# Kernel tuning notes

Hardware: AMD Instinct MI355X
Metric: run time of the kernel (lower is better)

## Reference

```python
import jax, jax.numpy as jnp
import numpy as np

C_IN, C_HID, N_HEADS = 128, 32, 4
INF = 1.0e9
LN_EPS = 1e-5


def setup_inputs() -> dict:
    key = jax.random.key(0)
    ks = jax.random.split(key, 12)
    B, I, J, C, H, D = 1, 384, 384, C_IN, N_HEADS, C_HID
    s = 0.02
    return {
        "x": jax.random.normal(ks[0], (B, I, J, C), dtype=jnp.float32),
        "mask": jnp.ones((B, I, J), dtype=jnp.float32),
        "ln_g": jnp.ones((C,), dtype=jnp.float32),
        "ln_b": jnp.zeros((C,), dtype=jnp.float32),
        "w_tri": jax.random.normal(ks[1], (C, H), dtype=jnp.float32) * s,
        "wq": jax.random.normal(ks[2], (C, H, D), dtype=jnp.float32) * s,
        "wk": jax.random.normal(ks[3], (C, H, D), dtype=jnp.float32) * s,
        "wv": jax.random.normal(ks[4], (C, H, D), dtype=jnp.float32) * s,
        "wg": jax.random.normal(ks[5], (C, H, D), dtype=jnp.float32) * s,
        "bg": jnp.ones((H, D), dtype=jnp.float32),
        "wo": jax.random.normal(ks[6], (H, D, C), dtype=jnp.float32) * s,
        "bo": jnp.zeros((C,), dtype=jnp.float32),
    }


def reference(x, mask, ln_g, ln_b, w_tri, wq, wk, wv, wg, bg, wo, bo):
    # LayerNorm over channel dim
    mu = jnp.mean(x, axis=-1, keepdims=True)
    var = jnp.mean(jnp.square(x - mu), axis=-1, keepdims=True)
    xn = (x - mu) * jax.lax.rsqrt(var + LN_EPS) * ln_g + ln_b  # [B,I,J,C]

    # mask bias: [B, I, 1, 1, J]
    mask_bias = (INF * (mask - 1.0))[..., :, None, None, :]
    # triangle bias: linear(x) -> [B,I,J,H] -> [B,1,H,I,J]
    tri_bias = jnp.einsum("bijc,ch->bhij", xn, w_tri)[:, None]

    scale = 1.0 / jnp.sqrt(jnp.asarray(C_HID, dtype=xn.dtype))
    # per-row attention over J: tensors [B, I, H, J, D]
    q = jnp.einsum("bixc,chd->bihxd", xn, wq) * scale
    k = jnp.einsum("bixc,chd->bihxd", xn, wk)
    v = jnp.einsum("bixc,chd->bihxd", xn, wv)

    logits = jnp.einsum("bihqd,bihkd->bihqk", q, k) + mask_bias + tri_bias
    a = jax.nn.softmax(logits, axis=-1)
    o = jnp.einsum("bihqk,bihkd->bihqd", a, v)  # [B,I,H,J,D]

    g = jax.nn.sigmoid(jnp.einsum("bixc,chd->bihxd", xn, wg) + bg[None, None, :, None, :])
    o = o * g
    out = jnp.einsum("bihxd,hdc->bixc", o, wo) + bo  # [B,I,J,C]
    return out
```

## Files before the change

### kernel.cpp

```cpp
#include <hip/hip_runtime.h>
#include <math.h>


#define I_DIM 384
#define J_DIM 384
#define C_DIM 128
#define H_DIM 4
#define D_DIM 32
#define NPOS (I_DIM * J_DIM)
#define Q_SCALE 0.17677669529663687f

typedef __attribute__((ext_vector_type(8))) short bf16x8;
typedef __attribute__((ext_vector_type(4))) float f32x4;

__device__ __forceinline__ float sigmoidf_(float v) {
    return 1.0f / (1.0f + __expf(-v));
}
__device__ __forceinline__ unsigned short f2bf(float f) {
    union { float f; unsigned u; } x; x.f = f;
    unsigned u = x.u;
    u += 0x7fffu + ((u >> 16) & 1u);
    return (unsigned short)(u >> 16);
}
__device__ __forceinline__ float bf2f(unsigned short v) {
    union { unsigned u; float f; } x; x.u = ((unsigned)v) << 16;
    return x.f;
}

__global__ __launch_bounds__(256) void prep_kernel(
    const float* __restrict__ wq, const float* __restrict__ wk,
    const float* __restrict__ wv, const float* __restrict__ wg,
    const float* __restrict__ wo, unsigned short* __restrict__ Wt)
{
    const int mat = blockIdx.x;
    const float* W = (mat == 0) ? wq : (mat == 1) ? wk : (mat == 2) ? wv
                    : (mat == 3) ? wg : wo;
    const float scale = (mat == 0) ? Q_SCALE : 1.0f;
    const int t = threadIdx.x;
    const int n = t >> 1, c0 = (t & 1) * 64;
#pragma unroll
    for (int u = 0; u < 8; ++u) {
        unsigned pk[4];
#pragma unroll
        for (int w = 0; w < 4; ++w) {
            const unsigned short a = f2bf(W[(size_t)(c0 + u * 8 + w * 2 + 0) * 128 + n] * scale);
            const unsigned short b = f2bf(W[(size_t)(c0 + u * 8 + w * 2 + 1) * 128 + n] * scale);
            pk[w] = (unsigned)a | ((unsigned)b << 16);
        }
        int4 q; q.x = pk[0]; q.y = pk[1]; q.z = pk[2]; q.w = pk[3];
        *(int4*)(Wt + (size_t)mat * 16384 + n * 128 + c0 + u * 8) = q;
    }
}

__global__ __launch_bounds__(256) void proj_kernel(
    const float* __restrict__ x, const float* __restrict__ ln_g,
    const float* __restrict__ ln_b, const float* __restrict__ w_tri,
    const unsigned short* __restrict__ Wt, const float* __restrict__ bg,
    unsigned short* __restrict__ qb, unsigned short* __restrict__ kb,
    unsigned short* __restrict__ vb, unsigned short* __restrict__ gb,
    float* __restrict__ tri)
{
    __shared__ unsigned short At[128 * 128];
    __shared__ unsigned short Bt[128 * 128];

    const int t = threadIdx.x;
    const int pos0 = blockIdx.x * 128;
    const int lane = t & 63, wave = t >> 6;
    const int q15 = lane & 15, quad = lane >> 4;

    {
        const int r = t >> 1, half = t & 1, c0 = half * 64;
        const float* xrow = x + (size_t)(pos0 + r) * C_DIM + c0;
        float xv[64];
        float s = 0.f, ss = 0.f;
#pragma unroll
        for (int u = 0; u < 16; ++u) {
            float4 v4 = ((const float4*)xrow)[u];
            xv[u * 4 + 0] = v4.x; xv[u * 4 + 1] = v4.y;
            xv[u * 4 + 2] = v4.z; xv[u * 4 + 3] = v4.w;
            s  += v4.x + v4.y + v4.z + v4.w;
            ss += v4.x * v4.x + v4.y * v4.y + v4.z * v4.z + v4.w * v4.w;
        }
        s  += __shfl_xor(s, 1);
        ss += __shfl_xor(ss, 1);
        const float mu  = s * (1.0f / 128.0f);
        const float var = ss * (1.0f / 128.0f) - mu * mu;
        const float rstd = rsqrtf(var + 1e-5f);

        float ptri[4] = {0.f, 0.f, 0.f, 0.f};
#pragma unroll
        for (int u = 0; u < 8; ++u) {
            const float4 g0 = ((const float4*)(ln_g + c0))[u * 2];
            const float4 g1 = ((const float4*)(ln_g + c0))[u * 2 + 1];
            const float4 b0 = ((const float4*)(ln_b + c0))[u * 2];
            const float4 b1 = ((const float4*)(ln_b + c0))[u * 2 + 1];
            float xn8[8];
            xn8[0] = (xv[u * 8 + 0] - mu) * rstd * g0.x + b0.x;
            xn8[1] = (xv[u * 8 + 1] - mu) * rstd * g0.y + b0.y;
            xn8[2] = (xv[u * 8 + 2] - mu) * rstd * g0.z + b0.z;
            xn8[3] = (xv[u * 8 + 3] - mu) * rstd * g0.w + b0.w;
            xn8[4] = (xv[u * 8 + 4] - mu) * rstd * g1.x + b1.x;
            xn8[5] = (xv[u * 8 + 5] - mu) * rstd * g1.y + b1.y;
            xn8[6] = (xv[u * 8 + 6] - mu) * rstd * g1.z + b1.z;
            xn8[7] = (xv[u * 8 + 7] - mu) * rstd * g1.w + b1.w;
#pragma unroll
            for (int w = 0; w < 8; ++w) {
                const float4 wt = ((const float4*)w_tri)[c0 + u * 8 + w];
                ptri[0] += xn8[w] * wt.x; ptri[1] += xn8[w] * wt.y;
                ptri[2] += xn8[w] * wt.z; ptri[3] += xn8[w] * wt.w;
            }
            unsigned pk[4];
#pragma unroll
            for (int w = 0; w < 4; ++w)
                pk[w] = (unsigned)f2bf(xn8[w * 2]) | ((unsigned)f2bf(xn8[w * 2 + 1]) << 16);
            int4 q4; q4.x = pk[0]; q4.y = pk[1]; q4.z = pk[2]; q4.w = pk[3];
            const int c = half * 8 + u;
            *(int4*)&At[r * 128 + ((c ^ (r & 7)) * 8)] = q4;
        }
#pragma unroll
        for (int hh = 0; hh < 4; ++hh) ptri[hh] += __shfl_xor(ptri[hh], 1);
        const int pos = pos0 + r;
        const int i = pos / J_DIM, j = pos - (pos / J_DIM) * J_DIM;
        const int h0 = half * 2;
        tri[((size_t)(h0 + 0) * J_DIM + j) * I_DIM + i] = ptri[h0 + 0];
        tri[((size_t)(h0 + 1) * J_DIM + j) * I_DIM + i] = ptri[h0 + 1];
    }

    const int m0 = wave * 32;
    for (int mat = 0; mat < 4; ++mat) {
        __syncthreads();
        {
            const int rn = t >> 1, half = t & 1;
            const unsigned short* src = Wt + (size_t)mat * 16384 + rn * 128 + half * 64;
#pragma unroll
            for (int u = 0; u < 8; ++u) {
                const int c = half * 8 + u;
                *(int4*)&Bt[rn * 128 + ((c ^ (rn & 7)) * 8)] = *(const int4*)(src + u * 8);
            }
        }
        __syncthreads();

        f32x4 acc[2][8];
#pragma unroll
        for (int mt = 0; mt < 2; ++mt)
#pragma unroll
            for (int nt = 0; nt < 8; ++nt) acc[mt][nt] = (f32x4){0.f, 0.f, 0.f, 0.f};

#pragma unroll
        for (int kk = 0; kk < 4; ++kk) {
            const int sw = ((kk * 4 + quad) ^ (q15 & 7)) * 8;
            const bf16x8 a0 = *(const bf16x8*)&At[(m0 + q15) * 128 + sw];
            const bf16x8 a1 = *(const bf16x8*)&At[(m0 + 16 + q15) * 128 + sw];
#pragma unroll
            for (int nt = 0; nt < 8; ++nt) {
                const bf16x8 b = *(const bf16x8*)&Bt[(nt * 16 + q15) * 128 + sw];
                acc[0][nt] = __builtin_amdgcn_mfma_f32_16x16x32_bf16(a0, b, acc[0][nt], 0, 0, 0);
                acc[1][nt] = __builtin_amdgcn_mfma_f32_16x16x32_bf16(a1, b, acc[1][nt], 0, 0, 0);
            }
        }

        __syncthreads();
#pragma unroll
        for (int mt = 0; mt < 2; ++mt)
#pragma unroll
            for (int nt = 0; nt < 8; ++nt) {
                const int col = nt * 16 + q15;
                const float bgl = (mat == 3) ? bg[col] : 0.f;
#pragma unroll
                for (int reg = 0; reg < 4; ++reg) {
                    float v = acc[mt][nt][reg];
                    if (mat == 3) v = sigmoidf_(v + bgl);
                    const int row = m0 + mt * 16 + quad * 4 + reg;
                    Bt[row * 128 + (((col >> 3) ^ (row & 7)) * 8) + (col & 7)] = f2bf(v);
                }
            }
        __syncthreads();
        {
            unsigned short* O = (mat == 0) ? qb : (mat == 1) ? kb : (mat == 2) ? vb : gb;
#pragma unroll
            for (int sgm = 0; sgm < 2; ++sgm) {
                const int ch = t + sgm * 256;
                const int r = ch >> 2, hh = ch & 3;
                const int pos = pos0 + r;
                const int i = pos / J_DIM, j = pos - (pos / J_DIM) * J_DIM;
                unsigned short* dst = O + (((size_t)i * H_DIM + hh) * J_DIM + j) * D_DIM;
#pragma unroll
                for (int w = 0; w < 4; ++w) {
                    const int c = hh * 4 + w;
                    *(int4*)(dst + w * 8) = *(const int4*)&Bt[r * 128 + ((c ^ (r & 7)) * 8)];
                }
            }
        }
    }
}

__global__ __launch_bounds__(256) void attn_kernel(
    const unsigned short* __restrict__ qb, const unsigned short* __restrict__ kb,
    const unsigned short* __restrict__ vb, unsigned short* gob,
    const float* __restrict__ triT, const float* __restrict__ mask)
{
    __shared__ unsigned short Klds[64 * 32];
    __shared__ unsigned short Vt[32 * 68];
    __shared__ unsigned short Plds[4][32 * 68];
    __shared__ float Mb[J_DIM];

    const int t = threadIdx.x;
    const int lane = t & 63, wave = t >> 6;
    const int q15 = lane & 15, quad = lane >> 4;
    const int i = blockIdx.x >> 2, h = blockIdx.x & 3;
    const size_t hb = (size_t)(i * H_DIM + h) * (J_DIM * D_DIM);
    const int m0 = wave * 96;

    for (int idx = t; idx < J_DIM; idx += 256)
        Mb[idx] = 1.0e9f * (mask[i * J_DIM + idx] - 1.0f);

    bf16x8 qf[6];
#pragma unroll
    for (int m = 0; m < 6; ++m)
        qf[m] = *(const bf16x8*)(qb + hb + (size_t)(m0 + m * 16 + q15) * D_DIM + quad * 8);

    f32x4 Oacc[6][2];
    float sums[6][4];
#pragma unroll
    for (int m = 0; m < 6; ++m) {
#pragma unroll
        for (int d2 = 0; d2 < 2; ++d2) Oacc[m][d2] = (f32x4){0.f, 0.f, 0.f, 0.f};
#pragma unroll
        for (int r = 0; r < 4; ++r) sums[m][r] = 0.f;
    }

    unsigned short* Pw = Plds[wave];
    const float* triH = triT + (size_t)h * J_DIM * I_DIM;

    for (int kt = 0; kt < 6; ++kt) {
        __syncthreads();
        {
            const int kp = t >> 2, du = (t & 3) * 8;
            const size_t gsrc = hb + (size_t)(kt * 64 + kp) * D_DIM + du;
            *(int4*)&Klds[kp * 32 + du] = *(const int4*)(kb + gsrc);
            int4 vv = *(const int4*)(vb + gsrc);
            const unsigned short* vs = (const unsigned short*)&vv;
#pragma unroll
            for (int u = 0; u < 8; ++u)
                Vt[(du + u) * 68 + kp] = vs[u];
        }
        __syncthreads();

        bf16x8 vf[2][2];
#pragma unroll
        for (int ks = 0; ks < 2; ++ks)
#pragma unroll
            for (int d2 = 0; d2 < 2; ++d2)
                vf[ks][d2] = *(const bf16x8*)&Vt[(d2 * 16 + q15) * 68 + ks * 32 + quad * 8];

#pragma unroll
        for (int pass = 0; pass < 3; ++pass) {
            const int mbase = pass * 2;

#pragma unroll
            for (int nt = 0; nt < 4; ++nt) {
                const bf16x8 kf = *(const bf16x8*)&Klds[(nt * 16 + q15) * 32 + quad * 8];
                const float mb = Mb[kt * 64 + nt * 16 + q15];
                const float* tcol = triH + (size_t)(kt * 64 + nt * 16 + q15) * I_DIM;
#pragma unroll
                for (int mm = 0; mm < 2; ++mm) {
                    const int m = mbase + mm;
                    const float4 tb = *(const float4*)(tcol + m0 + m * 16 + quad * 4);
                    f32x4 s = {0.f, 0.f, 0.f, 0.f};
                    s = __builtin_amdgcn_mfma_f32_16x16x32_bf16(qf[m], kf, s, 0, 0, 0);
                    const float p0 = __expf(s[0] + mb + tb.x);
                    const float p1 = __expf(s[1] + mb + tb.y);
                    const float p2 = __expf(s[2] + mb + tb.z);
                    const float p3 = __expf(s[3] + mb + tb.w);
                    sums[m][0] += p0; sums[m][1] += p1;
                    sums[m][2] += p2; sums[m][3] += p3;
                    const int row = mm * 16 + quad * 4;
                    const int col = nt * 16 + q15;
                    Pw[(row + 0) * 68 + col] = f2bf(p0);
                    Pw[(row + 1) * 68 + col] = f2bf(p1);
                    Pw[(row + 2) * 68 + col] = f2bf(p2);
                    Pw[(row + 3) * 68 + col] = f2bf(p3);
                }
            }

#pragma unroll
            for (int mm = 0; mm < 2; ++mm) {
                const int m = mbase + mm;
#pragma unroll
                for (int ks = 0; ks < 2; ++ks) {
                    const bf16x8 af = *(const bf16x8*)&Pw[(mm * 16 + q15) * 68 + ks * 32 + quad * 8];
                    Oacc[m][0] = __builtin_amdgcn_mfma_f32_16x16x32_bf16(af, vf[ks][0], Oacc[m][0], 0, 0, 0);
                    Oacc[m][1] = __builtin_amdgcn_mfma_f32_16x16x32_bf16(af, vf[ks][1], Oacc[m][1], 0, 0, 0);
                }
            }
        }
    }

    float inv[6][4];
#pragma unroll
    for (int m = 0; m < 6; ++m)
#pragma unroll
        for (int r = 0; r < 4; ++r) {
            float s0 = sums[m][r];
            s0 += __shfl_xor(s0, 1); s0 += __shfl_xor(s0, 2);
            s0 += __shfl_xor(s0, 4); s0 += __shfl_xor(s0, 8);
            inv[m][r] = 1.0f / s0;
        }

#pragma unroll
    for (int m = 0; m < 6; ++m) {
        const int qrow = m0 + m * 16 + quad * 4;
#pragma unroll
        for (int d2 = 0; d2 < 2; ++d2) {
            const int d = d2 * 16 + q15;
#pragma unroll
            for (int r = 0; r < 4; ++r) {
                const size_t idx = hb + (size_t)(qrow + r) * D_DIM + d;
                const float g = bf2f(gob[idx]);
                gob[idx] = f2bf(Oacc[m][d2][r] * inv[m][r] * g);
            }
        }
    }
}

__global__ __launch_bounds__(256) void out_kernel(
    const unsigned short* __restrict__ og, const unsigned short* __restrict__ WtO,
    const float* __restrict__ bo, float* __restrict__ out)
{
    __shared__ unsigned short At[128 * 128];
    __shared__ unsigned short Bt[128 * 128];

    const int t = threadIdx.x;
    const int pos0 = blockIdx.x * 128;
    const int lane = t & 63, wave = t >> 6;
    const int q15 = lane & 15, quad = lane >> 4;

    {
        const int r = t >> 1, half = t & 1;
        const int pos = pos0 + r;
        const int i = pos / J_DIM, j = pos - (pos / J_DIM) * J_DIM;
#pragma unroll
        for (int u = 0; u < 8; ++u) {
            const int k0 = half * 64 + u * 8;
            const int hh = k0 >> 5, d0 = k0 & 31;
            const int4 v = *(const int4*)(og + (((size_t)i * H_DIM + hh) * J_DIM + j) * D_DIM + d0);
            const int c = half * 8 + u;
            *(int4*)&At[r * 128 + ((c ^ (r & 7)) * 8)] = v;
        }
        const unsigned short* src = WtO + r * 128 + half * 64;
#pragma unroll
        for (int u = 0; u < 8; ++u) {
            const int c = half * 8 + u;
            *(int4*)&Bt[r * 128 + ((c ^ (r & 7)) * 8)] = *(const int4*)(src + u * 8);
        }
    }
    __syncthreads();

    const int m0 = wave * 32;
    f32x4 acc[2][8];
#pragma unroll
    for (int mt = 0; mt < 2; ++mt)
#pragma unroll
        for (int nt = 0; nt < 8; ++nt) acc[mt][nt] = (f32x4){0.f, 0.f, 0.f, 0.f};

#pragma unroll
    for (int kk = 0; kk < 4; ++kk) {
        const int sw = ((kk * 4 + quad) ^ (q15 & 7)) * 8;
        const bf16x8 a0 = *(const bf16x8*)&At[(m0 + q15) * 128 + sw];
        const bf16x8 a1 = *(const bf16x8*)&At[(m0 + 16 + q15) * 128 + sw];
#pragma unroll
        for (int nt = 0; nt < 8; ++nt) {
            const bf16x8 b = *(const bf16x8*)&Bt[(nt * 16 + q15) * 128 + sw];
            acc[0][nt] = __builtin_amdgcn_mfma_f32_16x16x32_bf16(a0, b, acc[0][nt], 0, 0, 0);
            acc[1][nt] = __builtin_amdgcn_mfma_f32_16x16x32_bf16(a1, b, acc[1][nt], 0, 0, 0);
        }
    }

#pragma unroll
    for (int mt = 0; mt < 2; ++mt)
#pragma unroll
        for (int nt = 0; nt < 8; ++nt) {
            const float bov = bo[nt * 16 + q15];
#pragma unroll
            for (int reg = 0; reg < 4; ++reg) {
                const int pos = pos0 + m0 + mt * 16 + quad * 4 + reg;
                out[(size_t)pos * C_DIM + nt * 16 + q15] = acc[mt][nt][reg] + bov;
            }
        }
}

extern "C" void kernel_launch(void* const* d_in, const int* in_sizes, int n_in,
                              void* d_out, int out_size, void* d_ws, size_t ws_size,
                              hipStream_t stream)
{
    const float* x     = (const float*)d_in[0];
    const float* mask  = (const float*)d_in[1];
    const float* ln_g  = (const float*)d_in[2];
    const float* ln_b  = (const float*)d_in[3];
    const float* w_tri = (const float*)d_in[4];
    const float* wq    = (const float*)d_in[5];
    const float* wk    = (const float*)d_in[6];
    const float* wv    = (const float*)d_in[7];
    const float* wg    = (const float*)d_in[8];
    const float* bg    = (const float*)d_in[9];
    const float* wo    = (const float*)d_in[10];
    const float* bo    = (const float*)d_in[11];
    float* out = (float*)d_out;
    char* ws = (char*)d_ws;

    const size_t NE = (size_t)NPOS * 128;
    unsigned short* qb = (unsigned short*)ws;
    unsigned short* kb = (unsigned short*)(ws + NE * 2);
    unsigned short* vb = (unsigned short*)(ws + NE * 4);
    unsigned short* gb = (unsigned short*)(ws + NE * 6);
    float*         tri = (float*)(ws + NE * 8);
    unsigned short* Wt = (unsigned short*)(ws + NE * 8 + (size_t)NPOS * 4 * 4);

    prep_kernel<<<5, 256, 0, stream>>>(wq, wk, wv, wg, wo, Wt);
    proj_kernel<<<NPOS / 128, 256, 0, stream>>>(x, ln_g, ln_b, w_tri, Wt, bg,
                                                qb, kb, vb, gb, tri);
    attn_kernel<<<I_DIM * H_DIM, 256, 0, stream>>>(qb, kb, vb, gb, tri, mask);
    out_kernel<<<NPOS / 128, 256, 0, stream>>>(gb, Wt + 4 * 16384, bo, out);
}
```

Baseline: 493.8 us.

## Read weights from global/L2 directly and shrink LDS to raise occupancy

Proj and out kernels no longer stage the 128x128 bf16 weight matrix in shared memory. MFMA B fragments are loaded straight from global memory, which should hit in cache. The proj epilogue now stages output through a small 128x32 buffer one head at a time, and the LayerNorm prologue uses four threads per row. Both kernels gain launch_bounds hints of 4 blocks per CU. The aim is to cut LDS use (64KB to about 40KB or 32KB) and several barriers so more blocks stay resident, at the cost of global-latency B loads inside the MFMA loop and more barriers in the epilogue.

Measured after the change: 537.8 us. +8.9%, slower.

```diff
diff --git a/kernel.cpp b/kernel.cpp
--- a/kernel.cpp
+++ b/kernel.cpp
@@ -52,7 +52,7 @@
     }
 }
 
-__global__ __launch_bounds__(256) void proj_kernel(
+__global__ __launch_bounds__(256, 4) void proj_kernel(
     const float* __restrict__ x, const float* __restrict__ ln_g,
     const float* __restrict__ ln_b, const float* __restrict__ w_tri,
     const unsigned short* __restrict__ Wt, const float* __restrict__ bg,
@@ -61,7 +61,7 @@
     float* __restrict__ tri)
 {
     __shared__ unsigned short At[128 * 128];
-    __shared__ unsigned short Bt[128 * 128];
+    __shared__ unsigned short Ct[128 * 32];
 
     const int t = threadIdx.x;
     const int pos0 = blockIdx.x * 128;
@@ -69,76 +69,73 @@
     const int q15 = lane & 15, quad = lane >> 4;
 
     {
-        const int r = t >> 1, half = t & 1, c0 = half * 64;
-        const float* xrow = x + (size_t)(pos0 + r) * C_DIM + c0;
-        float xv[64];
-        float s = 0.f, ss = 0.f;
-#pragma unroll
-        for (int u = 0; u < 16; ++u) {
-            float4 v4 = ((const float4*)xrow)[u];
-            xv[u * 4 + 0] = v4.x; xv[u * 4 + 1] = v4.y;
-            xv[u * 4 + 2] = v4.z; xv[u * 4 + 3] = v4.w;
-            s  += v4.x + v4.y + v4.z + v4.w;
-            ss += v4.x * v4.x + v4.y * v4.y + v4.z * v4.z + v4.w * v4.w;
-        }
-        s  += __shfl_xor(s, 1);
-        ss += __shfl_xor(ss, 1);
-        const float mu  = s * (1.0f / 128.0f);
-        const float var = ss * (1.0f / 128.0f) - mu * mu;
-        const float rstd = rsqrtf(var + 1e-5f);
-
-        float ptri[4] = {0.f, 0.f, 0.f, 0.f};
-#pragma unroll
-        for (int u = 0; u < 8; ++u) {
-            const float4 g0 = ((const float4*)(ln_g + c0))[u * 2];
-            const float4 g1 = ((const float4*)(ln_g + c0))[u * 2 + 1];
-            const float4 b0 = ((const float4*)(ln_b + c0))[u * 2];
-            const float4 b1 = ((const float4*)(ln_b + c0))[u * 2 + 1];
-            float xn8[8];
-            xn8[0] = (xv[u * 8 + 0] - mu) * rstd * g0.x + b0.x;
-            xn8[1] = (xv[u * 8 + 1] - mu) * rstd * g0.y + b0.y;
-            xn8[2] = (xv[u * 8 + 2] - mu) * rstd * g0.z + b0.z;
-            xn8[3] = (xv[u * 8 + 3] - mu) * rstd * g0.w + b0.w;
-            xn8[4] = (xv[u * 8 + 4] - mu) * rstd * g1.x + b1.x;
-            xn8[5] = (xv[u * 8 + 5] - mu) * rstd * g1.y + b1.y;
-            xn8[6] = (xv[u * 8 + 6] - mu) * rstd * g1.z + b1.z;
-            xn8[7] = (xv[u * 8 + 7] - mu) * rstd * g1.w + b1.w;
-#pragma unroll
-            for (int w = 0; w < 8; ++w) {
-                const float4 wt = ((const float4*)w_tri)[c0 + u * 8 + w];
-                ptri[0] += xn8[w] * wt.x; ptri[1] += xn8[w] * wt.y;
-                ptri[2] += xn8[w] * wt.z; ptri[3] += xn8[w] * wt.w;
-            }
-            unsigned pk[4];
-#pragma unroll
-            for (int w = 0; w < 4; ++w)
-                pk[w] = (unsigned)f2bf(xn8[w * 2]) | ((unsigned)f2bf(xn8[w * 2 + 1]) << 16);
-            int4 q4; q4.x = pk[0]; q4.y = pk[1]; q4.z = pk[2]; q4.w = pk[3];
-            const int c = half * 8 + u;
-            *(int4*)&At[r * 128 + ((c ^ (r & 7)) * 8)] = q4;
-        }
-#pragma unroll
-        for (int hh = 0; hh < 4; ++hh) ptri[hh] += __shfl_xor(ptri[hh], 1);
-        const int pos = pos0 + r;
-        const int i = pos / J_DIM, j = pos - (pos / J_DIM) * J_DIM;
-        const int h0 = half * 2;
-        tri[((size_t)(h0 + 0) * J_DIM + j) * I_DIM + i] = ptri[h0 + 0];
-        tri[((size_t)(h0 + 1) * J_DIM + j) * I_DIM + i] = ptri[h0 + 1];
-    }
+        const int g = t >> 2, q = t & 3;
+#pragma unroll
+        for (int rr = 0; rr < 2; ++rr) {
+            const int r = g * 2 + rr;
+            const float* xrow = x + (size_t)(pos0 + r) * C_DIM + q * 32;
+            float xv[32];
+            float s = 0.f, ss = 0.f;
+#pragma unroll
+            for (int u = 0; u < 8; ++u) {
+                float4 v4 = ((const float4*)xrow)[u];
+                xv[u * 4 + 0] = v4.x; xv[u * 4 + 1] = v4.y;
+                xv[u * 4 + 2] = v4.z; xv[u * 4 + 3] = v4.w;
+                s  += v4.x + v4.y + v4.z + v4.w;
+                ss += v4.x * v4.x + v4.y * v4.y + v4.z * v4.z + v4.w * v4.w;
+            }
+            s  += __shfl_xor(s, 1);  s  += __shfl_xor(s, 2);
+            ss += __shfl_xor(ss, 1); ss += __shfl_xor(ss, 2);
+            const float mu  = s * (1.0f / 128.0f);
+            const float var = ss * (1.0f / 128.0f) - mu * mu;
+            const float rstd = rsqrtf(var + 1e-5f);
+
+            float ptri[4] = {0.f, 0.f, 0.f, 0.f};
+#pragma unroll
+            for (int u2 = 0; u2 < 4; ++u2) {
+                const int cb = q * 32 + u2 * 8;
+                const float4 g0 = *(const float4*)(ln_g + cb);
+                const float4 g1 = *(const float4*)(ln_g + cb + 4);
+                const float4 b0 = *(const float4*)(ln_b + cb);
+                const float4 b1 = *(const float4*)(ln_b + cb + 4);
+                float xn8[8];
+                xn8[0] = (xv[u2 * 8 + 0] - mu) * rstd * g0.x + b0.x;
+                xn8[1] = (xv[u2 * 8 + 1] - mu) * rstd * g0.y + b0.y;
+                xn8[2] = (xv[u2 * 8 + 2] - mu) * rstd * g0.z + b0.z;
+                xn8[3] = (xv[u2 * 8 + 3] - mu) * rstd * g0.w + b0.w;
+                xn8[4] = (xv[u2 * 8 + 4] - mu) * rstd * g1.x + b1.x;
+                xn8[5] = (xv[u2 * 8 + 5] - mu) * rstd * g1.y + b1.y;
+                xn8[6] = (xv[u2 * 8 + 6] - mu) * rstd * g1.z + b1.z;
+                xn8[7] = (xv[u2 * 8 + 7] - mu) * rstd * g1.w + b1.w;
+#pragma unroll
+                for (int w = 0; w < 8; ++w) {
+                    const float4 wt = ((const float4*)w_tri)[cb + w];
+                    ptri[0] += xn8[w] * wt.x; ptri[1] += xn8[w] * wt.y;
+                    ptri[2] += xn8[w] * wt.z; ptri[3] += xn8[w] * wt.w;
+                }
+                unsigned pk[4];
+#pragma unroll
+                for (int w = 0; w < 4; ++w)
+                    pk[w] = (unsigned)f2bf(xn8[w * 2]) | ((unsigned)f2bf(xn8[w * 2 + 1]) << 16);
+                int4 q4; q4.x = pk[0]; q4.y = pk[1]; q4.z = pk[2]; q4.w = pk[3];
+                const int c = q * 4 + u2;
+                *(int4*)&At[r * 128 + ((c ^ (r & 7)) * 8)] = q4;
+            }
+#pragma unroll
+            for (int hh = 0; hh < 4; ++hh) {
+                ptri[hh] += __shfl_xor(ptri[hh], 1);
+                ptri[hh] += __shfl_xor(ptri[hh], 2);
+            }
+            const int pos = pos0 + r;
+            const int i = pos / J_DIM, j = pos - (pos / J_DIM) * J_DIM;
+            tri[((size_t)q * J_DIM + j) * I_DIM + i] = ptri[q];
+        }
+    }
+    __syncthreads();
 
     const int m0 = wave * 32;
     for (int mat = 0; mat < 4; ++mat) {
-        __syncthreads();
-        {
-            const int rn = t >> 1, half = t & 1;
-            const unsigned short* src = Wt + (size_t)mat * 16384 + rn * 128 + half * 64;
-#pragma unroll
-            for (int u = 0; u < 8; ++u) {
-                const int c = half * 8 + u;
-                *(int4*)&Bt[rn * 128 + ((c ^ (rn & 7)) * 8)] = *(const int4*)(src + u * 8);
-            }
-        }
-        __syncthreads();
+        const unsigned short* WtM = Wt + (size_t)mat * 16384;
 
         f32x4 acc[2][8];
 #pragma unroll
@@ -151,44 +148,45 @@
             const int sw = ((kk * 4 + quad) ^ (q15 & 7)) * 8;
             const bf16x8 a0 = *(const bf16x8*)&At[(m0 + q15) * 128 + sw];
             const bf16x8 a1 = *(const bf16x8*)&At[(m0 + 16 + q15) * 128 + sw];
+            const unsigned short* bp = WtM + q15 * 128 + (kk * 4 + quad) * 8;
 #pragma unroll
             for (int nt = 0; nt < 8; ++nt) {
-                const bf16x8 b = *(const bf16x8*)&Bt[(nt * 16 + q15) * 128 + sw];
+                const bf16x8 b = *(const bf16x8*)(bp + nt * 16 * 128);
                 acc[0][nt] = __builtin_amdgcn_mfma_f32_16x16x32_bf16(a0, b, acc[0][nt], 0, 0, 0);
                 acc[1][nt] = __builtin_amdgcn_mfma_f32_16x16x32_bf16(a1, b, acc[1][nt], 0, 0, 0);
             }
         }
 
-        __syncthreads();
-#pragma unroll
-        for (int mt = 0; mt < 2; ++mt)
-#pragma unroll
-            for (int nt = 0; nt < 8; ++nt) {
-                const int col = nt * 16 + q15;
-                const float bgl = (mat == 3) ? bg[col] : 0.f;
-#pragma unroll
-                for (int reg = 0; reg < 4; ++reg) {
-                    float v = acc[mt][nt][reg];
-                    if (mat == 3) v = sigmoidf_(v + bgl);
-                    const int row = m0 + mt * 16 + quad * 4 + reg;
-                    Bt[row * 128 + (((col >> 3) ^ (row & 7)) * 8) + (col & 7)] = f2bf(v);
+        unsigned short* O = (mat == 0) ? qb : (mat == 1) ? kb : (mat == 2) ? vb : gb;
+#pragma unroll
+        for (int qp = 0; qp < 4; ++qp) {
+            __syncthreads();
+#pragma unroll
+            for (int mt = 0; mt < 2; ++mt)
+#pragma unroll
+                for (int n2 = 0; n2 < 2; ++n2) {
+                    const int nt = qp * 2 + n2;
+                    const int lc = n2 * 16 + q15;
+                    const float bgl = (mat == 3) ? bg[qp * 32 + lc] : 0.f;
+#pragma unroll
+                    for (int reg = 0; reg < 4; ++reg) {
+                        float v = acc[mt][nt][reg];
+                        if (mat == 3) v = sigmoidf_(v + bgl);
+                        const int row = m0 + mt * 16 + quad * 4 + reg;
+                        const int cs = ((lc >> 3) ^ (row & 3) ^ ((row >> 2) & 3)) & 3;
+                        Ct[row * 32 + cs * 8 + (lc & 7)] = f2bf(v);
+                    }
                 }
-            }
-        __syncthreads();
-        {
-            unsigned short* O = (mat == 0) ? qb : (mat == 1) ? kb : (mat == 2) ? vb : gb;
-#pragma unroll
-            for (int sgm = 0; sgm < 2; ++sgm) {
-                const int ch = t + sgm * 256;
-                const int r = ch >> 2, hh = ch & 3;
+            __syncthreads();
+#pragma unroll
+            for (int s = 0; s < 2; ++s) {
+                const int ch = s * 256 + t;
+                const int r = ch >> 2, c = ch & 3;
+                const int cs = (c ^ (r & 3) ^ ((r >> 2) & 3)) & 3;
+                const int4 v = *(const int4*)&Ct[r * 32 + cs * 8];
                 const int pos = pos0 + r;
                 const int i = pos / J_DIM, j = pos - (pos / J_DIM) * J_DIM;
-                unsigned short* dst = O + (((size_t)i * H_DIM + hh) * J_DIM + j) * D_DIM;
-#pragma unroll
-                for (int w = 0; w < 4; ++w) {
-                    const int c = hh * 4 + w;
-                    *(int4*)(dst + w * 8) = *(const int4*)&Bt[r * 128 + ((c ^ (r & 7)) * 8)];
-                }
+                *(int4*)(O + (((size_t)i * H_DIM + qp) * J_DIM + j) * D_DIM + c * 8) = v;
             }
         }
     }
@@ -323,12 +321,11 @@
     }
 }
 
-__global__ __launch_bounds__(256) void out_kernel(
+__global__ __launch_bounds__(256, 4) void out_kernel(
     const unsigned short* __restrict__ og, const unsigned short* __restrict__ WtO,
     const float* __restrict__ bo, float* __restrict__ out)
 {
     __shared__ unsigned short At[128 * 128];
-    __shared__ unsigned short Bt[128 * 128];
 
     const int t = threadIdx.x;
     const int pos0 = blockIdx.x * 128;
@@ -347,12 +344,6 @@
             const int c = half * 8 + u;
             *(int4*)&At[r * 128 + ((c ^ (r & 7)) * 8)] = v;
         }
-        const unsigned short* src = WtO + r * 128 + half * 64;
-#pragma unroll
-        for (int u = 0; u < 8; ++u) {
-            const int c = half * 8 + u;
-            *(int4*)&Bt[r * 128 + ((c ^ (r & 7)) * 8)] = *(const int4*)(src + u * 8);
-        }
     }
     __syncthreads();
 
@@ -368,9 +359,10 @@
         const int sw = ((kk * 4 + quad) ^ (q15 & 7)) * 8;
         const bf16x8 a0 = *(const bf16x8*)&At[(m0 + q15) * 128 + sw];
         const bf16x8 a1 = *(const bf16x8*)&At[(m0 + 16 + q15) * 128 + sw];
+        const unsigned short* bp = WtO + q15 * 128 + (kk * 4 + quad) * 8;
 #pragma unroll
         for (int nt = 0; nt < 8; ++nt) {
-            const bf16x8 b = *(const bf16x8*)&Bt[(nt * 16 + q15) * 128 + sw];
+            const bf16x8 b = *(const bf16x8*)(bp + nt * 16 * 128);
             acc[0][nt] = __builtin_amdgcn_mfma_f32_16x16x32_bf16(a0, b, acc[0][nt], 0, 0, 0);
             acc[1][nt] = __builtin_amdgcn_mfma_f32_16x16x32_bf16(a1, b, acc[1][nt], 0, 0, 0);
         }
```
